# Kernel optimization log

Hardware: AMD Instinct MI355X
Metric: run time of the kernel (lower is better)

The kernel has to match this reference:

```python
import jax, jax.numpy as jnp
import numpy as np

N = 20000      # nodes
E = 320000     # edges
S = 256        # scalar (0e) channels of irreps_feature
F = 960        # full irreps_feature dim (256x0e+128x1e+64x2e)
NB = 32        # number_of_basis
CUT = 5.0      # max_radius


def setup_inputs() -> dict:
    key = jax.random.key(0)
    ks = jax.random.split(key, 24)
    def w(k, shape):
        return jax.random.normal(k, shape, jnp.float32) / np.sqrt(shape[0])
    return {
        "node_feature": jax.random.normal(ks[0], (N, F), jnp.float32),
        "pos": jax.random.normal(ks[1], (N, 3), jnp.float32),
        "edge_index": jax.random.randint(ks[2], (2, E), 0, N),
        "W_ai1": w(ks[3], (S, S)), "b_ai1": jnp.zeros((S,), jnp.float32),
        "W_ai2": w(ks[4], (S, 1)), "b_ai2": jnp.zeros((1,), jnp.float32),
        "W_ci1": w(ks[5], (S, S)), "b_ci1": jnp.zeros((S,), jnp.float32),
        "W_ci2": w(ks[6], (S, 1)), "b_ci2": jnp.zeros((1,), jnp.float32),
        "W_sc": w(ks[7], (S, S)), "b_sc": jnp.zeros((S,), jnp.float32),
        "W_ed": w(ks[8], (NB, S)), "b_ed": jnp.zeros((S,), jnp.float32),
        "W_b1": w(ks[9], (3 * S, S)), "b_b1": jnp.zeros((S,), jnp.float32),
        "W_b2": w(ks[10], (S, 1)), "b_b2": jnp.zeros((1,), jnp.float32),
    }


def _rbf(d):
    # ExpNormalSmearing (torchmd-net), cutoff_lower=0, cutoff_upper=CUT, non-trainable
    start = np.exp(-CUT)
    means = jnp.linspace(start, 1.0, NB, dtype=jnp.float32)
    beta = jnp.float32(((2.0 / NB) * (1.0 - start)) ** -2)
    cosine_cut = 0.5 * (jnp.cos(np.pi * d / CUT) + 1.0) * (d < CUT)
    return cosine_cut[:, None] * jnp.exp(-beta * (jnp.exp(-d)[:, None] - means) ** 2)


def reference(node_feature, pos, edge_index,
              W_ai1, b_ai1, W_ai2, b_ai2,
              W_ci1, b_ci1, W_ci2, b_ci2,
              W_sc, b_sc, W_ed, b_ed,
              W_b1, b_b1, W_b2, b_b2):
    # LinearRS(irreps_feature -> 0e) only touches the 0e block (first S channels)
    scal = node_feature[:, :S]
    silu = jax.nn.silu

    log_ai = silu(scal @ W_ai1 + b_ai1) @ W_ai2 + b_ai2          # [N,1]
    ai = jnp.exp(log_ai)
    log_ci = silu(scal @ W_ci1 + b_ci1) @ W_ci2 + b_ci2          # [N,1]
    ci = jnp.exp(log_ci)

    src, dst = edge_index[0], edge_index[1]
    rel = pos[dst] - pos[src]                                     # [E,3]
    norm = jnp.linalg.norm(rel, axis=1, keepdims=True)            # [E,1]
    rhat = rel / (norm + 1e-8)
    emb = _rbf(norm[:, 0])                                        # [E,NB]

    node_sc = scal @ W_sc + b_sc                                  # project once, gather [N,S]
    src_f = node_sc[src]
    dst_f = node_sc[dst]
    edge_f = emb @ W_ed + b_ed
    edge_feature = jnp.concatenate([src_f, dst_f, edge_f], axis=-1)  # [E,3S]
    bij = silu(edge_feature @ W_b1 + b_b1) @ W_b2 + b_b2          # [E,1]

    # edge softmax over incoming edges of dst, with extra ci mass
    bmax = jax.ops.segment_max(bij, dst, num_segments=N)
    bmax = jnp.where(jnp.isneginf(bmax), 0.0, bmax)
    bij_exp = jnp.exp(bij - bmax[dst])
    bsum = jax.ops.segment_sum(bij_exp, dst, num_segments=N) + ci  # [N,1]
    gamma = bij_exp / (bsum[dst] + 1e-7)                           # [E,1]

    bij_prime = gamma * ai[dst]                                    # [E,1]
    outer = rhat[:, :, None] * rhat[:, None, :]                    # [E,3,3]
    contrib = jax.ops.segment_sum(bij_prime[:, :, None] * outer, dst, num_segments=N)  # [N,3,3]

    eye3 = jnp.eye(3, dtype=pos.dtype)
    sigma = ai[:, :, None] * eye3 - contrib + 1e-6 * eye3          # [N,3,3]
    sum_gamma = jax.ops.segment_sum(gamma, dst, num_segments=N)    # [N,1]
    return sigma, ai, sum_gamma
```

## Files before the change

### kernel.cpp

```cpp
#include <hip/hip_runtime.h>
#include <math.h>

#define N_NODES 20000
#define E_EDGES 320000
#define F_DIM   960
#define S_DIM   256
#define QTAB    2048
#define ASTRIDE 264
#define CAP     64

typedef __attribute__((ext_vector_type(8))) short short8;
typedef __attribute__((ext_vector_type(4))) float f32x4;
typedef _Float16 half8 __attribute__((ext_vector_type(8)));

__device__ __forceinline__ float siluf(float x) {
    return x / (1.0f + __expf(-x));
}

__device__ __forceinline__ unsigned short bf16rn(float x) {
    unsigned u = __float_as_uint(x);
    return (unsigned short)((u + 0x7FFFu + ((u >> 16) & 1u)) >> 16);
}

__device__ __forceinline__ void bf16x8_to_f32(short8 v8, float* o) {
    union { short8 s; uint4 u; } cv; cv.s = v8;
    o[0] = __uint_as_float(cv.u.x << 16);
    o[1] = __uint_as_float(cv.u.x & 0xffff0000u);
    o[2] = __uint_as_float(cv.u.y << 16);
    o[3] = __uint_as_float(cv.u.y & 0xffff0000u);
    o[4] = __uint_as_float(cv.u.z << 16);
    o[5] = __uint_as_float(cv.u.z & 0xffff0000u);
    o[6] = __uint_as_float(cv.u.w << 16);
    o[7] = __uint_as_float(cv.u.w & 0xffff0000u);
}

__global__ void prep_kernel(const float* __restrict__ W_sc, const float* __restrict__ W_ed,
                            const float* __restrict__ W_b1, const float* __restrict__ b_sc,
                            const float* __restrict__ b_ed, const float* __restrict__ b_b1,
                            const float* __restrict__ W_ai1, const float* __restrict__ W_ci1,
                            float* __restrict__ Bcat, float* __restrict__ We, float* __restrict__ c0,
                            int* __restrict__ cnt)
{
    int idx = blockIdx.x * 256 + threadIdx.x;
    if (idx < N_NODES) cnt[idx] = 0;
    if (idx < 256 * 1024) {
        int k = idx >> 10, j = idx & 1023;
        float s = 0.0f;
        if (j < 256) {
            for (int m = 0; m < 256; ++m) s += W_sc[k * 256 + m] * W_b1[m * 256 + j];
        } else if (j < 512) {
            int jj = j - 256;
            for (int m = 0; m < 256; ++m) s += W_sc[k * 256 + m] * W_b1[(256 + m) * 256 + jj];
        } else if (j < 768) {
            s = W_ai1[k * 256 + (j - 512)];
        } else {
            s = W_ci1[k * 256 + (j - 768)];
        }
        Bcat[idx] = s;
    } else if (idx < 256 * 1024 + 32 * 256) {
        int t = idx - 256 * 1024;
        int p = t >> 8, j = t & 255;
        float s = 0.0f;
        for (int m = 0; m < 256; ++m) s += W_ed[p * 256 + m] * W_b1[(512 + m) * 256 + j];
        We[t] = s;
    } else if (idx < 256 * 1024 + 32 * 256 + 256) {
        int j = idx - 256 * 1024 - 32 * 256;
        float s = b_b1[j];
        for (int m = 0; m < 256; ++m) {
            s += b_sc[m] * (W_b1[m * 256 + j] + W_b1[(256 + m) * 256 + j]);
            s += b_ed[m] * W_b1[(512 + m) * 256 + j];
        }
        c0[j] = s;
    }
}

__global__ void aux_kernel(const int* __restrict__ ei, int* __restrict__ cnt, int* __restrict__ rank,
                           const float* __restrict__ Bcat, unsigned short* __restrict__ Bpack,
                           const float* __restrict__ We, _Float16* __restrict__ Tab,
                           const float* __restrict__ nf, unsigned short* __restrict__ scalp)
{
    int b = blockIdx.x;
    if (b < 1250) {
        int i = b * 256 + threadIdx.x;
        rank[i] = atomicAdd(&cnt[ei[E_EDGES + i]], 1);
    } else if (b < 1378) {
        int idx = (b - 1250) * 256 + threadIdx.x;
        int kq = idx & 3, j = (idx >> 2) & 1023, t = idx >> 12;
        #pragma unroll
        for (int jj = 0; jj < 8; ++jj)
            Bpack[idx * 8 + jj] = bf16rn(Bcat[(t * 32 + kq * 8 + jj) * 1024 + j]);
    } else if (b < 3426) {
        int idx = (b - 1378) * 256 + threadIdx.x;
        int q = idx >> 8, j = idx & 255;
        float nrm = 5.0f * (float)q / (float)(QTAB - 1);
        const float start = 0.006737946999085467f;
        const float mustep = (1.0f - start) / 31.0f;
        const float bx = (2.0f / 32.0f) * (1.0f - start);
        const float beta = 1.0f / (bx * bx);
        const float PI_F = 3.14159265358979323846f;
        float cc = (nrm < 5.0f) ? 0.5f * (__cosf(PI_F * nrm * 0.2f) + 1.0f) : 0.0f;
        float t = __expf(-nrm);
        float s = 0.0f;
        for (int k = 0; k < 32; ++k) {
            float dm = t - (start + (float)k * mustep);
            s += __expf(-beta * dm * dm) * We[k * 256 + j];
        }
        Tab[idx] = (_Float16)(cc * s);
    } else {
        int idx = (b - 3426) * 256 + threadIdx.x;
        int base = idx * 4;
        int n = base >> 8, k = base & 255;
        float4 a4 = *(const float4*)&nf[(size_t)n * F_DIM + k];
        ushort4 b4;
        b4.x = bf16rn(a4.x); b4.y = bf16rn(a4.y);
        b4.z = bf16rn(a4.z); b4.w = bf16rn(a4.w);
        *(ushort4*)&scalp[n * 256 + k] = b4;
    }
}

__global__ __launch_bounds__(1024) void scan_kernel(const int* __restrict__ cnt,
                                                    int* __restrict__ start)
{
    extern __shared__ int ls[];
    __shared__ int ps[1024];
    const int t = threadIdx.x;
    for (int i = t; i < N_NODES; i += 1024) ls[i] = cnt[i];
    __syncthreads();

    const int base = t * 20;
    int loc[20];
    int s = 0;
    #pragma unroll
    for (int i = 0; i < 20; ++i) {
        int n = (base + i < N_NODES) ? ls[base + i] : 0;
        loc[i] = s; s += n;
    }
    ps[t] = s;
    __syncthreads();
    for (int off = 1; off < 1024; off <<= 1) {
        int v = (t >= off) ? ps[t - off] : 0;
        __syncthreads();
        ps[t] += v;
        __syncthreads();
    }
    int offset = ps[t] - s;
    #pragma unroll
    for (int i = 0; i < 20; ++i)
        if (base + i < N_NODES) ls[base + i] = offset + loc[i];
    __syncthreads();
    for (int i = t; i < N_NODES; i += 1024) start[i] = ls[i];
}

__global__ void scatter_kernel(const int* __restrict__ ei, const int* __restrict__ start,
                               const int* __restrict__ rank, int2* __restrict__ sd)
{
    int i = blockIdx.x * 256 + threadIdx.x;
    if (i < E_EDGES) {
        int d = ei[E_EDGES + i];
        int2 p; p.x = ei[i]; p.y = d;
        sd[start[d] + rank[i]] = p;
    }
}

__global__ __launch_bounds__(256) void node_mfma_kernel(
    const unsigned short* __restrict__ scalp, const unsigned short* __restrict__ Bpack,
    const float* __restrict__ c0,
    const float* __restrict__ b_ai1, const float* __restrict__ W_ai2, const float* __restrict__ b_ai2,
    const float* __restrict__ b_ci1, const float* __restrict__ W_ci2, const float* __restrict__ b_ci2,
    _Float16* __restrict__ u, _Float16* __restrict__ v,
    float* __restrict__ bsumseed, float* __restrict__ out_ai)
{
    __shared__ unsigned short A[32 * ASTRIDE];
    __shared__ float red[32 * 4];

    const int tid = threadIdx.x;
    const int w = tid >> 6, lane = tid & 63;
    const int bg = blockIdx.x & 3;
    const int m0 = (blockIdx.x >> 2) * 32;
    const int col16 = lane & 15, quad = lane >> 4;

    #pragma unroll
    for (int it = 0; it < 4; ++it) {
        int idx = (it * 256 + tid) * 8;
        int r = idx >> 8, c = idx & 255;
        *(uint4*)&A[r * ASTRIDE + c] = *(const uint4*)&scalp[(m0 + r) * 256 + c];
    }
    __syncthreads();

    f32x4 acc[2][4];
    #pragma unroll
    for (int mt = 0; mt < 2; ++mt)
        #pragma unroll
        for (int nt = 0; nt < 4; ++nt)
            acc[mt][nt] = (f32x4){0.0f, 0.0f, 0.0f, 0.0f};

    const int colbase = bg * 256 + w * 64;

    for (int t = 0; t < 8; ++t) {
        short8 af[2];
        #pragma unroll
        for (int mt = 0; mt < 2; ++mt)
            af[mt] = *(const short8*)&A[(mt * 16 + col16) * ASTRIDE + t * 32 + quad * 8];
        short8 bf[4];
        #pragma unroll
        for (int nt = 0; nt < 4; ++nt)
            bf[nt] = *(const short8*)&Bpack[(((t * 1024 + colbase + nt * 16 + col16) * 4) + quad) * 8];
        #pragma unroll
        for (int mt = 0; mt < 2; ++mt)
            #pragma unroll
            for (int nt = 0; nt < 4; ++nt)
                acc[mt][nt] = __builtin_amdgcn_mfma_f32_16x16x32_bf16(af[mt], bf[nt], acc[mt][nt], 0, 0, 0);
    }

    if (bg == 0) {
        #pragma unroll
        for (int nt = 0; nt < 4; ++nt) {
            int jl = w * 64 + nt * 16 + col16;
            float c0v = c0[jl];
            #pragma unroll
            for (int mt = 0; mt < 2; ++mt)
                #pragma unroll
                for (int reg = 0; reg < 4; ++reg)
                    u[(m0 + mt * 16 + quad * 4 + reg) * 256 + jl] = (_Float16)(acc[mt][nt][reg] + c0v);
        }
    } else if (bg == 1) {
        #pragma unroll
        for (int nt = 0; nt < 4; ++nt) {
            int jl = w * 64 + nt * 16 + col16;
            #pragma unroll
            for (int mt = 0; mt < 2; ++mt)
                #pragma unroll
                for (int reg = 0; reg < 4; ++reg)
                    v[(m0 + mt * 16 + quad * 4 + reg) * 256 + jl] = (_Float16)(acc[mt][nt][reg]);
        }
    } else {
        const float* b1 = (bg == 2) ? b_ai1 : b_ci1;
        const float* w2 = (bg == 2) ? W_ai2 : W_ci2;
        float s[2][4] = {{0, 0, 0, 0}, {0, 0, 0, 0}};
        #pragma unroll
        for (int nt = 0; nt < 4; ++nt) {
            int jl = w * 64 + nt * 16 + col16;
            float bb = b1[jl], ww = w2[jl];
            #pragma unroll
            for (int mt = 0; mt < 2; ++mt)
                #pragma unroll
                for (int reg = 0; reg < 4; ++reg)
                    s[mt][reg] += siluf(acc[mt][nt][reg] + bb) * ww;
        }
        #pragma unroll
        for (int off = 1; off < 16; off <<= 1) {
            #pragma unroll
            for (int mt = 0; mt < 2; ++mt)
                #pragma unroll
                for (int reg = 0; reg < 4; ++reg)
                    s[mt][reg] += __shfl_xor(s[mt][reg], off);
        }
        if (col16 == 0) {
            #pragma unroll
            for (int mt = 0; mt < 2; ++mt)
                #pragma unroll
                for (int reg = 0; reg < 4; ++reg)
                    red[(mt * 16 + quad * 4 + reg) * 4 + w] = s[mt][reg];
        }
        __syncthreads();
        if (tid < 32) {
            float sum = red[tid * 4] + red[tid * 4 + 1] + red[tid * 4 + 2] + red[tid * 4 + 3];
            if (bg == 2) out_ai[m0 + tid] = expf(sum + b_ai2[0]);
            else         bsumseed[m0 + tid] = expf(sum + b_ci2[0]) + 1e-7f;
        }
    }
}

__global__ __launch_bounds__(256) void edge_bij_kernel(
    const int2* __restrict__ sd, const float* __restrict__ pos,
    const _Float16* __restrict__ u, const _Float16* __restrict__ v,
    const _Float16* __restrict__ Tab,
    const float* __restrict__ W_b2, const float* __restrict__ b_b2,
    float4* __restrict__ bijS)
{
    const int l = threadIdx.x & 15;
    const int slot = blockIdx.x * 16 + (threadIdx.x >> 4);
    const int2 e = sd[slot];
    const int src = e.x;
    const int dst = e.y;

    float px = pos[3 * dst + 0] - pos[3 * src + 0];
    float py = pos[3 * dst + 1] - pos[3 * src + 1];
    float pz = pos[3 * dst + 2] - pos[3 * src + 2];
    float nrm = sqrtf(px * px + py * py + pz * pz);
    float inv = 1.0f / (nrm + 1e-8f);
    float rx = px * inv, ry = py * inv, rz = pz * inv;

    const float xscale = (float)(QTAB - 1) * 0.2f;
    float x = nrm * xscale;
    int qi = (int)x;
    float f = x - (float)qi;
    if (qi >= QTAB - 1) { qi = QTAB - 2; f = 1.0f; }
    const _Float16 fh = (_Float16)f;

    float w2c[16];
    #pragma unroll
    for (int c = 0; c < 16; c += 4)
        *(float4*)&w2c[c] = *(const float4*)&W_b2[l * 16 + c];

    const unsigned lo = (unsigned)l * 32u;
    const char* ub = (const char*)u + ((unsigned)src * 512u + lo);
    const char* vb = (const char*)v + ((unsigned)dst * 512u + lo);
    const char* tb = (const char*)Tab + ((unsigned)qi * 512u + lo);

    half8 u0 = *(const half8*)(ub);
    half8 u1 = *(const half8*)(ub + 16);
    half8 v0 = *(const half8*)(vb);
    half8 v1 = *(const half8*)(vb + 16);
    half8 t00 = *(const half8*)(tb);
    half8 t01 = *(const half8*)(tb + 16);
    half8 t10 = *(const half8*)(tb + 512);
    half8 t11 = *(const half8*)(tb + 528);

    half8 h0 = (u0 + v0) + (t00 + fh * (t10 - t00));
    half8 h1 = (u1 + v1) + (t01 + fh * (t11 - t01));

    float acc = 0.0f;
    #pragma unroll
    for (int c = 0; c < 8; ++c) {
        float hf = (float)h0[c];
        float sig = __builtin_amdgcn_rcpf(1.0f + __expf(-hf));
        acc += w2c[c] * hf * sig;
    }
    #pragma unroll
    for (int c = 0; c < 8; ++c) {
        float hf = (float)h1[c];
        float sig = __builtin_amdgcn_rcpf(1.0f + __expf(-hf));
        acc += w2c[8 + c] * hf * sig;
    }
    #pragma unroll
    for (int off = 1; off < 16; off <<= 1) acc += __shfl_xor(acc, off);

    if (l == 0) {
        float4 o;
        o.x = acc + b_b2[0];
        o.y = rx; o.z = ry; o.w = rz;
        bijS[slot] = o;
    }
}

__global__ __launch_bounds__(256) void node_reduce_kernel(
    const int* __restrict__ start, const int* __restrict__ cnt,
    const float4* __restrict__ bijS,
    const float* __restrict__ bsumseed, const float* __restrict__ out_ai,
    float* __restrict__ out_sigma, float* __restrict__ out_sg)
{
    const int grp = threadIdx.x >> 4;
    const int l = threadIdx.x & 15;
    const int g = blockIdx.x * 16 + grp;
    const int st = start[g];
    const int deg = min(cnt[g], CAP);

    float bj[4], ex[4], ey[4], ez[4];
    bool ok[4];
    float m = -1e30f;
    #pragma unroll
    for (int k = 0; k < 4; ++k) {
        int i = l + k * 16;
        ok[k] = (i < deg);
        float4 o;
        if (ok[k]) o = bijS[st + i];
        else { o.x = -1e30f; o.y = 0.0f; o.z = 0.0f; o.w = 0.0f; }
        bj[k] = o.x; ex[k] = o.y; ey[k] = o.z; ez[k] = o.w;
        m = fmaxf(m, bj[k]);
    }
    #pragma unroll
    for (int off = 1; off < 16; off <<= 1) m = fmaxf(m, __shfl_xor(m, off));

    float g4[4];
    float ssum = 0.0f;
    #pragma unroll
    for (int k = 0; k < 4; ++k) {
        g4[k] = ok[k] ? __expf(bj[k] - m) : 0.0f;
        ssum += g4[k];
    }
    #pragma unroll
    for (int off = 1; off < 16; off <<= 1) ssum += __shfl_xor(ssum, off);

    float invt = 1.0f / (ssum + bsumseed[g]);

    float a0 = 0, a1 = 0, a2 = 0, a3 = 0, a4 = 0, a5 = 0, a6 = 0;
    #pragma unroll
    for (int k = 0; k < 4; ++k) {
        float gm = g4[k] * invt;
        a0 += gm * ex[k] * ex[k]; a1 += gm * ey[k] * ey[k]; a2 += gm * ez[k] * ez[k];
        a3 += gm * ex[k] * ey[k]; a4 += gm * ex[k] * ez[k]; a5 += gm * ey[k] * ez[k];
        a6 += gm;
    }
    #pragma unroll
    for (int off = 1; off < 16; off <<= 1) {
        a0 += __shfl_xor(a0, off); a1 += __shfl_xor(a1, off);
        a2 += __shfl_xor(a2, off); a3 += __shfl_xor(a3, off);
        a4 += __shfl_xor(a4, off); a5 += __shfl_xor(a5, off);
        a6 += __shfl_xor(a6, off);
    }

    if (l == 0) {
        float ai = out_ai[g];
        float* sg = &out_sigma[g * 9];
        float d0 = ai + 1e-6f;
        sg[0] = d0 - ai * a0;
        sg[1] = -ai * a3;
        sg[2] = -ai * a4;
        sg[3] = -ai * a3;
        sg[4] = d0 - ai * a1;
        sg[5] = -ai * a5;
        sg[6] = -ai * a4;
        sg[7] = -ai * a5;
        sg[8] = d0 - ai * a2;
        out_sg[g] = a6;
    }
}

extern "C" void kernel_launch(void* const* d_in, const int* in_sizes, int n_in,
                              void* d_out, int out_size, void* d_ws, size_t ws_size,
                              hipStream_t stream)
{
    const float* nf    = (const float*)d_in[0];
    const float* pos   = (const float*)d_in[1];
    const int*   ei    = (const int*)  d_in[2];
    const float* W_ai1 = (const float*)d_in[3];
    const float* b_ai1 = (const float*)d_in[4];
    const float* W_ai2 = (const float*)d_in[5];
    const float* b_ai2 = (const float*)d_in[6];
    const float* W_ci1 = (const float*)d_in[7];
    const float* b_ci1 = (const float*)d_in[8];
    const float* W_ci2 = (const float*)d_in[9];
    const float* b_ci2 = (const float*)d_in[10];
    const float* W_sc  = (const float*)d_in[11];
    const float* b_sc  = (const float*)d_in[12];
    const float* W_ed  = (const float*)d_in[13];
    const float* b_ed  = (const float*)d_in[14];
    const float* W_b1  = (const float*)d_in[15];
    const float* b_b1  = (const float*)d_in[16];
    const float* W_b2  = (const float*)d_in[17];
    const float* b_b2  = (const float*)d_in[18];

    char* pb = (char*)d_ws;
    auto alloc = [&](size_t bytes) -> void* {
        void* r = (void*)pb;
        pb += (bytes + 255) & ~(size_t)255;
        return r;
    };
    float*          Bcat    = (float*)         alloc(262144 * 4);
    float*          We      = (float*)         alloc(8192 * 4);
    float*          c0      = (float*)         alloc(256 * 4);
    _Float16*       Tab     = (_Float16*)      alloc((size_t)QTAB * 256 * 2);
    unsigned short* Bpack   = (unsigned short*)alloc((size_t)256 * 1024 * 2);
    unsigned short* scalp   = (unsigned short*)alloc((size_t)N_NODES * 256 * 2);
    _Float16*       u       = (_Float16*)      alloc((size_t)N_NODES * 256 * 2);
    _Float16*       v       = (_Float16*)      alloc((size_t)N_NODES * 256 * 2);
    float*          bsumseed= (float*)         alloc((size_t)N_NODES * 4);
    int*            cnt     = (int*)           alloc((size_t)N_NODES * 4);
    int*            startA  = (int*)           alloc((size_t)N_NODES * 4);
    int*            rank    = (int*)           alloc((size_t)E_EDGES * 4);
    int2*           sd      = (int2*)          alloc((size_t)E_EDGES * 8);
    float4*         bijS    = (float4*)        alloc((size_t)E_EDGES * 16);

    float* out       = (float*)d_out;
    float* out_sigma = out;
    float* out_ai    = out + N_NODES * 9;
    float* out_sg    = out + N_NODES * 10;

    prep_kernel<<<1058, 256, 0, stream>>>(W_sc, W_ed, W_b1, b_sc, b_ed, b_b1, W_ai1, W_ci1,
                                          Bcat, We, c0, cnt);
    aux_kernel<<<8426, 256, 0, stream>>>(ei, cnt, rank, Bcat, Bpack, We, Tab, nf, scalp);
    scan_kernel<<<1, 1024, (size_t)N_NODES * 4, stream>>>(cnt, startA);
    scatter_kernel<<<1250, 256, 0, stream>>>(ei, startA, rank, sd);
    node_mfma_kernel<<<2500, 256, 0, stream>>>(scalp, Bpack, c0, b_ai1, W_ai2, b_ai2,
                                               b_ci1, W_ci2, b_ci2, u, v, bsumseed, out_ai);
    edge_bij_kernel<<<20000, 256, 0, stream>>>(sd, pos, u, v, Tab, W_b2, b_b2, bijS);
    node_reduce_kernel<<<1250, 256, 0, stream>>>(startA, cnt, bijS, bsumseed, out_ai,
                                                 out_sigma, out_sg);
}
```

Baseline: 287.3 us.

## Move edge geometry into scatter pass and halve node GEMM grid

Edge geometry (unit direction and scaled distance) is now computed in the scatter kernel and written to a CSR-ordered float4 buffer. The bij kernel only reads the table coordinate from it and writes a scalar bij, and the reduce kernel reads direction and bij separately. Separately, the node MFMA kernel now handles two column groups per block from a single A tile load, halving the grid. The aim is to move pos gathers out of the heavy edge kernel and reuse the staged A tile, at the cost of an extra geometry buffer round trip and less parallelism in the node GEMM.

After: 286.5 us. No clear change (-0.3%).

```diff
diff --git a/kernel.cpp b/kernel.cpp
--- a/kernel.cpp
+++ b/kernel.cpp
@@ -20,18 +20,6 @@
 __device__ __forceinline__ unsigned short bf16rn(float x) {
     unsigned u = __float_as_uint(x);
     return (unsigned short)((u + 0x7FFFu + ((u >> 16) & 1u)) >> 16);
-}
-
-__device__ __forceinline__ void bf16x8_to_f32(short8 v8, float* o) {
-    union { short8 s; uint4 u; } cv; cv.s = v8;
-    o[0] = __uint_as_float(cv.u.x << 16);
-    o[1] = __uint_as_float(cv.u.x & 0xffff0000u);
-    o[2] = __uint_as_float(cv.u.y << 16);
-    o[3] = __uint_as_float(cv.u.y & 0xffff0000u);
-    o[4] = __uint_as_float(cv.u.z << 16);
-    o[5] = __uint_as_float(cv.u.z & 0xffff0000u);
-    o[6] = __uint_as_float(cv.u.w << 16);
-    o[7] = __uint_as_float(cv.u.w & 0xffff0000u);
 }
 
 __global__ void prep_kernel(const float* __restrict__ W_sc, const float* __restrict__ W_ed,
@@ -151,15 +139,27 @@
     for (int i = t; i < N_NODES; i += 1024) start[i] = ls[i];
 }
 
-__global__ void scatter_kernel(const int* __restrict__ ei, const int* __restrict__ start,
-                               const int* __restrict__ rank, int2* __restrict__ sd)
+__global__ void edge_geom_kernel(const int* __restrict__ ei, const int* __restrict__ start,
+                                 const int* __restrict__ rank, const float* __restrict__ pos,
+                                 int2* __restrict__ sd, float4* __restrict__ geom)
 {
     int i = blockIdx.x * 256 + threadIdx.x;
-    if (i < E_EDGES) {
-        int d = ei[E_EDGES + i];
-        int2 p; p.x = ei[i]; p.y = d;
-        sd[start[d] + rank[i]] = p;
-    }
+    if (i >= E_EDGES) return;
+    int s = ei[i];
+    int d = ei[E_EDGES + i];
+    int slot = start[d] + rank[i];
+    int2 p; p.x = s; p.y = d;
+    sd[slot] = p;
+
+    float px = pos[3 * d + 0] - pos[3 * s + 0];
+    float py = pos[3 * d + 1] - pos[3 * s + 1];
+    float pz = pos[3 * d + 2] - pos[3 * s + 2];
+    float nrm = sqrtf(px * px + py * py + pz * pz);
+    float inv = 1.0f / (nrm + 1e-8f);
+    float4 o;
+    o.x = px * inv; o.y = py * inv; o.z = pz * inv;
+    o.w = nrm * (float)(QTAB - 1) * 0.2f;
+    geom[slot] = o;
 }
 
 __global__ __launch_bounds__(256) void node_mfma_kernel(
@@ -175,8 +175,8 @@
 
     const int tid = threadIdx.x;
     const int w = tid >> 6, lane = tid & 63;
-    const int bg = blockIdx.x & 3;
-    const int m0 = (blockIdx.x >> 2) * 32;
+    const int bg = blockIdx.x & 1;
+    const int m0 = (blockIdx.x >> 1) * 32;
     const int col16 = lane & 15, quad = lane >> 4;
 
     #pragma unroll
@@ -187,112 +187,108 @@
     }
     __syncthreads();
 
-    f32x4 acc[2][4];
-    #pragma unroll
-    for (int mt = 0; mt < 2; ++mt)
-        #pragma unroll
-        for (int nt = 0; nt < 4; ++nt)
-            acc[mt][nt] = (f32x4){0.0f, 0.0f, 0.0f, 0.0f};
-
-    const int colbase = bg * 256 + w * 64;
-
-    for (int t = 0; t < 8; ++t) {
-        short8 af[2];
+    for (int cc = 0; cc < 2; ++cc) {
+        const int cg = bg * 2 + cc;
+        f32x4 acc[2][4];
         #pragma unroll
         for (int mt = 0; mt < 2; ++mt)
-            af[mt] = *(const short8*)&A[(mt * 16 + col16) * ASTRIDE + t * 32 + quad * 8];
-        short8 bf[4];
-        #pragma unroll
-        for (int nt = 0; nt < 4; ++nt)
-            bf[nt] = *(const short8*)&Bpack[(((t * 1024 + colbase + nt * 16 + col16) * 4) + quad) * 8];
-        #pragma unroll
-        for (int mt = 0; mt < 2; ++mt)
             #pragma unroll
             for (int nt = 0; nt < 4; ++nt)
-                acc[mt][nt] = __builtin_amdgcn_mfma_f32_16x16x32_bf16(af[mt], bf[nt], acc[mt][nt], 0, 0, 0);
-    }
-
-    if (bg == 0) {
-        #pragma unroll
-        for (int nt = 0; nt < 4; ++nt) {
-            int jl = w * 64 + nt * 16 + col16;
-            float c0v = c0[jl];
+                acc[mt][nt] = (f32x4){0.0f, 0.0f, 0.0f, 0.0f};
+
+        const int colbase = cg * 256 + w * 64;
+
+        for (int t = 0; t < 8; ++t) {
+            short8 af[2];
             #pragma unroll
             for (int mt = 0; mt < 2; ++mt)
-                #pragma unroll
-                for (int reg = 0; reg < 4; ++reg)
-                    u[(m0 + mt * 16 + quad * 4 + reg) * 256 + jl] = (_Float16)(acc[mt][nt][reg] + c0v);
-        }
-    } else if (bg == 1) {
-        #pragma unroll
-        for (int nt = 0; nt < 4; ++nt) {
-            int jl = w * 64 + nt * 16 + col16;
+                af[mt] = *(const short8*)&A[(mt * 16 + col16) * ASTRIDE + t * 32 + quad * 8];
+            short8 bf[4];
+            #pragma unroll
+            for (int nt = 0; nt < 4; ++nt)
+                bf[nt] = *(const short8*)&Bpack[(((t * 1024 + colbase + nt * 16 + col16) * 4) + quad) * 8];
             #pragma unroll
             for (int mt = 0; mt < 2; ++mt)
                 #pragma unroll
-                for (int reg = 0; reg < 4; ++reg)
-                    v[(m0 + mt * 16 + quad * 4 + reg) * 256 + jl] = (_Float16)(acc[mt][nt][reg]);
-        }
-    } else {
-        const float* b1 = (bg == 2) ? b_ai1 : b_ci1;
-        const float* w2 = (bg == 2) ? W_ai2 : W_ci2;
-        float s[2][4] = {{0, 0, 0, 0}, {0, 0, 0, 0}};
-        #pragma unroll
-        for (int nt = 0; nt < 4; ++nt) {
-            int jl = w * 64 + nt * 16 + col16;
-            float bb = b1[jl], ww = w2[jl];
-            #pragma unroll
-            for (int mt = 0; mt < 2; ++mt)
-                #pragma unroll
-                for (int reg = 0; reg < 4; ++reg)
-                    s[mt][reg] += siluf(acc[mt][nt][reg] + bb) * ww;
-        }
-        #pragma unroll
-        for (int off = 1; off < 16; off <<= 1) {
-            #pragma unroll
-            for (int mt = 0; mt < 2; ++mt)
-                #pragma unroll
-                for (int reg = 0; reg < 4; ++reg)
-                    s[mt][reg] += __shfl_xor(s[mt][reg], off);
-        }
-        if (col16 == 0) {
-            #pragma unroll
-            for (int mt = 0; mt < 2; ++mt)
-                #pragma unroll
-                for (int reg = 0; reg < 4; ++reg)
-                    red[(mt * 16 + quad * 4 + reg) * 4 + w] = s[mt][reg];
-        }
-        __syncthreads();
-        if (tid < 32) {
-            float sum = red[tid * 4] + red[tid * 4 + 1] + red[tid * 4 + 2] + red[tid * 4 + 3];
-            if (bg == 2) out_ai[m0 + tid] = expf(sum + b_ai2[0]);
-            else         bsumseed[m0 + tid] = expf(sum + b_ci2[0]) + 1e-7f;
+                for (int nt = 0; nt < 4; ++nt)
+                    acc[mt][nt] = __builtin_amdgcn_mfma_f32_16x16x32_bf16(af[mt], bf[nt], acc[mt][nt], 0, 0, 0);
+        }
+
+        if (cg == 0) {
+            #pragma unroll
+            for (int nt = 0; nt < 4; ++nt) {
+                int jl = w * 64 + nt * 16 + col16;
+                float c0v = c0[jl];
+                #pragma unroll
+                for (int mt = 0; mt < 2; ++mt)
+                    #pragma unroll
+                    for (int reg = 0; reg < 4; ++reg)
+                        u[(m0 + mt * 16 + quad * 4 + reg) * 256 + jl] = (_Float16)(acc[mt][nt][reg] + c0v);
+        }
+        } else if (cg == 1) {
+            #pragma unroll
+            for (int nt = 0; nt < 4; ++nt) {
+                int jl = w * 64 + nt * 16 + col16;
+                #pragma unroll
+                for (int mt = 0; mt < 2; ++mt)
+                    #pragma unroll
+                    for (int reg = 0; reg < 4; ++reg)
+                        v[(m0 + mt * 16 + quad * 4 + reg) * 256 + jl] = (_Float16)(acc[mt][nt][reg]);
+            }
+        } else {
+            const float* b1 = (cg == 2) ? b_ai1 : b_ci1;
+            const float* w2 = (cg == 2) ? W_ai2 : W_ci2;
+            float s[2][4] = {{0, 0, 0, 0}, {0, 0, 0, 0}};
+            #pragma unroll
+            for (int nt = 0; nt < 4; ++nt) {
+                int jl = w * 64 + nt * 16 + col16;
+                float bb = b1[jl], ww = w2[jl];
+                #pragma unroll
+                for (int mt = 0; mt < 2; ++mt)
+                    #pragma unroll
+                    for (int reg = 0; reg < 4; ++reg)
+                        s[mt][reg] += siluf(acc[mt][nt][reg] + bb) * ww;
+            }
+            #pragma unroll
+            for (int off = 1; off < 16; off <<= 1) {
+                #pragma unroll
+                for (int mt = 0; mt < 2; ++mt)
+                    #pragma unroll
+                    for (int reg = 0; reg < 4; ++reg)
+                        s[mt][reg] += __shfl_xor(s[mt][reg], off);
+            }
+            if (col16 == 0) {
+                #pragma unroll
+                for (int mt = 0; mt < 2; ++mt)
+                    #pragma unroll
+                    for (int reg = 0; reg < 4; ++reg)
+                        red[(mt * 16 + quad * 4 + reg) * 4 + w] = s[mt][reg];
+            }
+            __syncthreads();
+            if (tid < 32) {
+                float sum = red[tid * 4] + red[tid * 4 + 1] + red[tid * 4 + 2] + red[tid * 4 + 3];
+                if (cg == 2) out_ai[m0 + tid] = expf(sum + b_ai2[0]);
+                else         bsumseed[m0 + tid] = expf(sum + b_ci2[0]) + 1e-7f;
+            }
+            __syncthreads();
         }
     }
 }
 
 __global__ __launch_bounds__(256) void edge_bij_kernel(
-    const int2* __restrict__ sd, const float* __restrict__ pos,
+    const int2* __restrict__ sd, const float4* __restrict__ geom,
     const _Float16* __restrict__ u, const _Float16* __restrict__ v,
     const _Float16* __restrict__ Tab,
     const float* __restrict__ W_b2, const float* __restrict__ b_b2,
-    float4* __restrict__ bijS)
+    float* __restrict__ bijV)
 {
     const int l = threadIdx.x & 15;
     const int slot = blockIdx.x * 16 + (threadIdx.x >> 4);
     const int2 e = sd[slot];
     const int src = e.x;
     const int dst = e.y;
-
-    float px = pos[3 * dst + 0] - pos[3 * src + 0];
-    float py = pos[3 * dst + 1] - pos[3 * src + 1];
-    float pz = pos[3 * dst + 2] - pos[3 * src + 2];
-    float nrm = sqrtf(px * px + py * py + pz * pz);
-    float inv = 1.0f / (nrm + 1e-8f);
-    float rx = px * inv, ry = py * inv, rz = pz * inv;
-
-    const float xscale = (float)(QTAB - 1) * 0.2f;
-    float x = nrm * xscale;
+    const float x = ((const float*)&geom[slot])[3];
+
     int qi = (int)x;
     float f = x - (float)qi;
     if (qi >= QTAB - 1) { qi = QTAB - 2; f = 1.0f; }
@@ -336,17 +332,12 @@
     #pragma unroll
     for (int off = 1; off < 16; off <<= 1) acc += __shfl_xor(acc, off);
 
-    if (l == 0) {
-        float4 o;
-        o.x = acc + b_b2[0];
-        o.y = rx; o.z = ry; o.w = rz;
-        bijS[slot] = o;
-    }
+    if (l == 0) bijV[slot] = acc + b_b2[0];
 }
 
 __global__ __launch_bounds__(256) void node_reduce_kernel(
     const int* __restrict__ start, const int* __restrict__ cnt,
-    const float4* __restrict__ bijS,
+    const float* __restrict__ bijV, const float4* __restrict__ geom,
     const float* __restrict__ bsumseed, const float* __restrict__ out_ai,
     float* __restrict__ out_sigma, float* __restrict__ out_sg)
 {
@@ -363,10 +354,13 @@
     for (int k = 0; k < 4; ++k) {
         int i = l + k * 16;
         ok[k] = (i < deg);
-        float4 o;
-        if (ok[k]) o = bijS[st + i];
-        else { o.x = -1e30f; o.y = 0.0f; o.z = 0.0f; o.w = 0.0f; }
-        bj[k] = o.x; ex[k] = o.y; ey[k] = o.z; ez[k] = o.w;
+        if (ok[k]) {
+            float4 o = geom[st + i];
+            bj[k] = bijV[st + i];
+            ex[k] = o.x; ey[k] = o.y; ez[k] = o.z;
+        } else {
+            bj[k] = -1e30f; ex[k] = 0.0f; ey[k] = 0.0f; ez[k] = 0.0f;
+        }
         m = fmaxf(m, bj[k]);
     }
     #pragma unroll
@@ -460,7 +454,8 @@
     int*            startA  = (int*)           alloc((size_t)N_NODES * 4);
     int*            rank    = (int*)           alloc((size_t)E_EDGES * 4);
     int2*           sd      = (int2*)          alloc((size_t)E_EDGES * 8);
-    float4*         bijS    = (float4*)        alloc((size_t)E_EDGES * 16);
+    float4*         geom    = (float4*)        alloc((size_t)E_EDGES * 16);
+    float*          bijV    = (float*)         alloc((size_t)E_EDGES * 4);
 
     float* out       = (float*)d_out;
     float* out_sigma = out;
@@ -471,10 +466,10 @@
                                           Bcat, We, c0, cnt);
     aux_kernel<<<8426, 256, 0, stream>>>(ei, cnt, rank, Bcat, Bpack, We, Tab, nf, scalp);
     scan_kernel<<<1, 1024, (size_t)N_NODES * 4, stream>>>(cnt, startA);
-    scatter_kernel<<<1250, 256, 0, stream>>>(ei, startA, rank, sd);
-    node_mfma_kernel<<<2500, 256, 0, stream>>>(scalp, Bpack, c0, b_ai1, W_ai2, b_ai2,
+    edge_geom_kernel<<<1250, 256, 0, stream>>>(ei, startA, rank, pos, sd, geom);
+    node_mfma_kernel<<<1250, 256, 0, stream>>>(scalp, Bpack, c0, b_ai1, W_ai2, b_ai2,
                                                b_ci1, W_ci2, b_ci2, u, v, bsumseed, out_ai);
-    edge_bij_kernel<<<20000, 256, 0, stream>>>(sd, pos, u, v, Tab, W_b2, b_b2, bijS);
-    node_reduce_kernel<<<1250, 256, 0, stream>>>(startA, cnt, bijS, bsumseed, out_ai,
+    edge_bij_kernel<<<20000, 256, 0, stream>>>(sd, geom, u, v, Tab, W_b2, b_b2, bijV);
+    node_reduce_kernel<<<1250, 256, 0, stream>>>(startA, cnt, bijV, geom, bsumseed, out_ai,
                                                  out_sigma, out_sg);
 }
```
